# Kernel tuning notes

Hardware: AMD Instinct MI355X
Metric: run time of the kernel (lower is better)

Reference implementation:

```python
import jax, jax.numpy as jnp
import numpy as np

C_IN = 512      # in_channels
C1 = 256        # inter_channels (theta/phi)
C2 = 512        # context_channels (g) -- must equal C_IN (forward views with in_channels)
H = W = 97      # feature map size == hardcoded pos-encoding grid
POS = 97
BN_EPS = 1e-5


def _pos_encoding():
    """Faithful numpy port of _POSITION_ENCODEING_INIT_SINCOS(1, 97, 97, C_IN//2).
    Returns [1, C_IN, 97, 97] float32 (NCHW)."""
    d = C_IN // 2
    i = np.arange(d)
    div = np.power(10000.0, 2 * (i // 2) / d)            # [d]
    pos_x = np.linspace(0, 10, POS)                       # outer dim (dim 1 of NHWC)
    pos_y = np.linspace(0, 20, POS)                       # inner dim (dim 2 of NHWC)
    a = np.broadcast_to(pos_y[None, :, None] / div, (POS, POS, d))  # pos_y terms
    b = np.broadcast_to(pos_x[:, None, None] / div, (POS, POS, d))  # pos_x terms
    enc = np.concatenate([a, b], axis=-1).copy()          # [97, 97, 2d]
    enc[..., 0::2] = np.sin(enc[..., 0::2])
    enc[..., 1::2] = np.cos(enc[..., 1::2])
    return np.transpose(enc, (2, 0, 1)).astype(np.float32)[None]  # [1, C_IN, 97, 97]


def _conv1x1(x, w, b):
    # 1x1 conv as channel GEMM: w [O, C], x [B, C, H, W]
    return jnp.einsum('oc,bchw->bohw', w, x) + b[None, :, None, None]


def _bn_inf(x, gamma, beta):
    # InPlaceABNSync(activation='none') in inference: running_mean=0, running_var=1
    inv = (1.0 / np.sqrt(1.0 + BN_EPS)).astype(np.float32)
    return x * (gamma * inv)[None, :, None, None] + beta[None, :, None, None]


def setup_inputs() -> dict:
    key = jax.random.key(0)
    ks = jax.random.split(key, 8)
    s = 0.05
    return {
        'x':           jax.random.normal(ks[0], (1, C_IN, H, W), jnp.float32),
        'pos':         jnp.asarray(_pos_encoding()),                      # [1, C_IN, 97, 97]
        'w_theta':     jax.random.normal(ks[1], (C1, 2 * C_IN), jnp.float32) * s,
        'b_theta':     jax.random.normal(ks[2], (C1,), jnp.float32) * s,
        'gamma_theta': 1.0 + jax.random.normal(ks[3], (C1,), jnp.float32) * s,
        'beta_theta':  jax.random.normal(ks[4], (C1,), jnp.float32) * s,
        'w_g':         jax.random.normal(ks[5], (C2, 2 * C_IN), jnp.float32) * s,
        'b_g':         jax.random.normal(ks[6], (C2,), jnp.float32) * s,
        'w_out':       jax.random.normal(ks[7], (C_IN, C2), jnp.float32) * s,
        'b_out':       jnp.zeros((C_IN,), jnp.float32),
    }


def reference(x, pos, w_theta, b_theta, gamma_theta, beta_theta, w_g, b_g, w_out, b_out):
    B, _, h, w = x.shape
    c1 = w_theta.shape[0]
    c2 = w_g.shape[0]
    # concat fuse of input with (shared) positional encoding
    pos_b = jnp.broadcast_to(pos, (B,) + pos.shape[1:])
    x_mix = jnp.concatenate([x, pos_b], axis=1)                 # [B, 2C, H, W]
    # theta == phi (shared weights), so f = theta^T theta
    t = jax.nn.relu(_bn_inf(_conv1x1(x_mix, w_theta, b_theta), gamma_theta, beta_theta))
    tn = t.reshape(B, c1, h * w)                                # [B, c1, N]
    f = jnp.einsum('bcn,bcm->bnm', tn, tn) * (c1 ** -0.5)       # [B, N, N]
    G = jax.nn.softmax(f, axis=-1)
    g = _conv1x1(x_mix, w_g, b_g).reshape(B, c2, h * w)         # [B, c2, N]
    y = jnp.einsum('bnm,bcm->bcn', G, g).reshape(B, c2, h, w)   # value aggregation
    return _conv1x1(y, w_out, b_out)                            # [B, C_IN, H, W]
```

## Files before the change

### kernel.cpp

```cpp
#include <hip/hip_runtime.h>
#include <hip/hip_bf16.h>


#define NTOK 9409
#define NP   9472
#define C1V  256
#define C2V  512
#define KD   1024
#define BN_INV 0.9999950000374997f

typedef _Float16 f16;
typedef _Float16 f16x8 __attribute__((ext_vector_type(8)));
typedef _Float16 f16x4 __attribute__((ext_vector_type(4)));
typedef _Float16 f16x2 __attribute__((ext_vector_type(2)));
typedef float    f32x4 __attribute__((ext_vector_type(4)));

typedef const __attribute__((address_space(1))) unsigned int* gp_t;
typedef __attribute__((address_space(3))) unsigned int* lp_t;
#define GLOAD_LDS16(gsrc, ldst) \
  __builtin_amdgcn_global_load_lds((gp_t)(const void*)(gsrc), (lp_t)(void*)(ldst), 16, 0, 0)

__global__ __launch_bounds__(256) void cvt_w_kernel(
    const float* __restrict__ wt, const float* __restrict__ bt,
    const float* __restrict__ gam, const float* __restrict__ bet,
    const float* __restrict__ wg, const float* __restrict__ wo,
    f16* __restrict__ wt16, f16* __restrict__ wg16, f16* __restrict__ wo16,
    float* __restrict__ btf) {
  if (blockIdx.x == 1024) {
    int o = threadIdx.x;
    btf[o] = bt[o] * (gam[o] * BN_INV) + bet[o];
    return;
  }
  int i4 = (blockIdx.x * 256 + threadIdx.x) * 4;
  if (i4 < 262144) {
    float4 v = *(const float4*)(wt + i4);
    float s = gam[i4 >> 10] * BN_INV;
    f16x4 o; o[0]=(f16)(v.x*s); o[1]=(f16)(v.y*s); o[2]=(f16)(v.z*s); o[3]=(f16)(v.w*s);
    *(f16x4*)(wt16 + i4) = o;
  } else if (i4 < 262144 + 524288) {
    int j = i4 - 262144;
    float4 v = *(const float4*)(wg + j);
    f16x4 o; o[0]=(f16)v.x; o[1]=(f16)v.y; o[2]=(f16)v.z; o[3]=(f16)v.w;
    *(f16x4*)(wg16 + j) = o;
  } else {
    int j = i4 - 786432;
    float4 v = *(const float4*)(wo + j);
    f16x4 o; o[0]=(f16)v.x; o[1]=(f16)v.y; o[2]=(f16)v.z; o[3]=(f16)v.w;
    *(f16x4*)(wo16 + j) = o;
  }
}

__global__ __launch_bounds__(256) void xpose_kernel(
    const float* __restrict__ x, const float* __restrict__ pos,
    f16* __restrict__ xT) {
  __shared__ f16 tile[64 * 68];
  const int k0 = blockIdx.x * 64;
  const int n0 = blockIdx.y * 64;
  const int tid = threadIdx.x;
  {
    const int kl = tid >> 4;
    const int nl = (tid & 15) * 4;
#pragma unroll
    for (int i = 0; i < 4; ++i) {
      int k = k0 + i * 16 + kl;
      const float* src = (k < 512) ? (x + (size_t)k * NTOK) : (pos + (size_t)(k - 512) * NTOK);
#pragma unroll
      for (int dd = 0; dd < 4; ++dd) {
        int n = n0 + nl + dd;
        float v = (n < NTOK) ? src[n] : 0.f;
        tile[(nl + dd) * 68 + i * 16 + kl] = (f16)v;
      }
    }
  }
  __syncthreads();
  {
    const int nl = tid >> 2;
    const int kc = (tid & 3) * 16;
    const int n = n0 + nl;
    f16x4 a = *(const f16x4*)(tile + nl * 68 + kc);
    f16x4 b = *(const f16x4*)(tile + nl * 68 + kc + 4);
    f16x4 c = *(const f16x4*)(tile + nl * 68 + kc + 8);
    f16x4 d = *(const f16x4*)(tile + nl * 68 + kc + 12);
    f16x8 v0, v1;
#pragma unroll
    for (int jj = 0; jj < 4; ++jj) { v0[jj] = a[jj]; v0[4 + jj] = b[jj]; v1[jj] = c[jj]; v1[4 + jj] = d[jj]; }
    if (n >= NTOK) {
#pragma unroll
      for (int jj = 0; jj < 8; ++jj) { v0[jj] = (f16)0.f; v1[jj] = (f16)0.f; }
    }
    f16* dst = xT + (size_t)n * KD + k0 + kc;
    *(f16x8*)(dst) = v0;
    *(f16x8*)(dst + 8) = v1;
  }
}

__global__ __launch_bounds__(256) void proj_theta_kernel(
    const f16* __restrict__ xT, const f16* __restrict__ wt16,
    const float* __restrict__ btf, f16* __restrict__ tT) {
  const int n0 = blockIdx.x * 128;
  const int o0 = blockIdx.y * 64;
  const int tid = threadIdx.x;
  const int w = tid >> 6, lane = tid & 63, l15 = lane & 15, l4 = lane >> 4;
  const int nb = n0 + w * 32;
  f32x4 acc[2][4];
#pragma unroll
  for (int i = 0; i < 2; ++i)
#pragma unroll
    for (int j = 0; j < 4; ++j) acc[i][j] = (f32x4){0.f,0.f,0.f,0.f};
  const f16* ap0 = xT + (size_t)(nb + l15) * KD + l4 * 8;
  const f16* bp  = wt16 + (size_t)(o0 + l15) * KD + l4 * 8;
#pragma unroll 2
  for (int k0 = 0; k0 < KD; k0 += 32) {
    f16x8 a0 = *(const f16x8*)(ap0 + k0);
    f16x8 a1 = *(const f16x8*)(ap0 + 16 * KD + k0);
    f16x8 b[4];
#pragma unroll
    for (int fo = 0; fo < 4; ++fo) b[fo] = *(const f16x8*)(bp + fo * 16 * KD + k0);
#pragma unroll
    for (int fo = 0; fo < 4; ++fo) {
      acc[0][fo] = __builtin_amdgcn_mfma_f32_16x16x32_f16(a0, b[fo], acc[0][fo], 0, 0, 0);
      acc[1][fo] = __builtin_amdgcn_mfma_f32_16x16x32_f16(a1, b[fo], acc[1][fo], 0, 0, 0);
    }
  }
#pragma unroll
  for (int fm = 0; fm < 2; ++fm)
#pragma unroll
    for (int fo = 0; fo < 4; ++fo) {
      int o = o0 + fo * 16 + l15;
      float bb = btf[o];
#pragma unroll
      for (int j = 0; j < 4; ++j) {
        int n = nb + fm * 16 + l4 * 4 + j;
        tT[(size_t)n * C1V + o] = (f16)fmaxf(acc[fm][fo][j] + bb, 0.f);
      }
    }
}

__global__ __launch_bounds__(256) void proj_g_kernel(
    const f16* __restrict__ xT, const f16* __restrict__ wg16,
    const float* __restrict__ bg, f16* __restrict__ gc) {
  const int n0 = blockIdx.x * 128;
  const int c0 = blockIdx.y * 128;
  const int tid = threadIdx.x;
  const int w = tid >> 6, lane = tid & 63, l15 = lane & 15, l4 = lane >> 4;
  const int cb = c0 + (w >> 1) * 64, nb = n0 + (w & 1) * 64;
  f32x4 acc[4][4];
#pragma unroll
  for (int i = 0; i < 4; ++i)
#pragma unroll
    for (int j = 0; j < 4; ++j) acc[i][j] = (f32x4){0.f,0.f,0.f,0.f};
  const f16* ap = wg16 + (size_t)(cb + l15) * KD + l4 * 8;
  const f16* bp = xT + (size_t)(nb + l15) * KD + l4 * 8;
  for (int k0 = 0; k0 < KD; k0 += 32) {
    f16x8 a[4], b[4];
#pragma unroll
    for (int fc = 0; fc < 4; ++fc) a[fc] = *(const f16x8*)(ap + fc * 16 * KD + k0);
#pragma unroll
    for (int fn = 0; fn < 4; ++fn) b[fn] = *(const f16x8*)(bp + fn * 16 * KD + k0);
#pragma unroll
    for (int fc = 0; fc < 4; ++fc)
#pragma unroll
      for (int fn = 0; fn < 4; ++fn)
        acc[fc][fn] = __builtin_amdgcn_mfma_f32_16x16x32_f16(a[fc], b[fn], acc[fc][fn], 0, 0, 0);
  }
#pragma unroll
  for (int fc = 0; fc < 4; ++fc)
#pragma unroll
    for (int j = 0; j < 4; ++j) {
      int c = cb + fc * 16 + l4 * 4 + j;
      float bb = bg[c];
#pragma unroll
      for (int fn = 0; fn < 4; ++fn) {
        int n = nb + fn * 16 + l15;
        gc[(size_t)c * NP + n] = (f16)(acc[fc][fn][j] + bb);
      }
    }
}

__global__ __launch_bounds__(512, 2) void attn_kernel(
    const f16* __restrict__ tT, const f16* __restrict__ gc,
    f16* __restrict__ part, float* __restrict__ stats) {
  __shared__ char lds[65536 + 9216 + 1024];
  f16* Pb = (f16*)(lds + 65536);
  float* MhL = (float*)(lds + 65536 + 9216);
  float* LhL = (float*)(lds + 65536 + 9216 + 512);
  const int bid = blockIdx.x;
  const int rb = bid >> 2, q = bid & 3;
  const int tid = threadIdx.x;
  const int w = tid >> 6, lane = tid & 63, l15 = lane & 15, l4 = lane >> 4;
  const int wr = (w & 3) * 16;
  const int mh = w >> 2;
  const int cs = w * 64;

  f16x8 Qf[8];
  {
    const f16* qp = tT + (size_t)(rb * 64 + wr + l15) * C1V + l4 * 8;
#pragma unroll
    for (int kk = 0; kk < 8; ++kk) Qf[kk] = *(const f16x8*)(qp + kk * 32);
  }

  f32x4 acc[4][4];
#pragma unroll
  for (int cf = 0; cf < 4; ++cf)
#pragma unroll
    for (int rf = 0; rf < 4; ++rf) acc[cf][rf] = (f32x4){0.f,0.f,0.f,0.f};
  float Mq[4] = {-1e30f,-1e30f,-1e30f,-1e30f}, Lq[4] = {0.f,0.f,0.f,0.f};
  float Mp[4] = {-1e30f,-1e30f,-1e30f,-1e30f}, Lp[4] = {0.f,0.f,0.f,0.f};

#define KPREF(tt, dstbase)                                        \
  {                                                               \
    const f16* kb_ = tT + (size_t)(tt) * 64 * C1V;                \
    _Pragma("unroll")                                             \
    for (int i_ = 0; i_ < 4; ++i_) {                              \
      int m_ = w * 8 + i_ * 2 + (lane >> 5);                      \
      int s_ = lane & 31;                                         \
      GLOAD_LDS16(kb_ + m_ * C1V + ((s_ ^ (m_ & 7)) << 3),        \
                  (dstbase) + (w * 4 + i_) * 1024);               \
    }                                                             \
  }

  const int tt0 = q * 37;
  KPREF(tt0, lds)
  __syncthreads();

  const f16* vp = gc + (size_t)(cs + l15) * NP + l4 * 8;
  const int krow0 = (mh * 32 + l15) * 512;

  for (int ti = 0; ti < 37; ++ti) {
    const int tt = tt0 + ti;
    const int m0 = tt * 64;
    const int cur = ti & 1;
    f16x8 vf0[4], vf1[4];
#pragma unroll
    for (int cf = 0; cf < 4; ++cf) vf0[cf] = *(const f16x8*)(vp + (size_t)cf * 16 * NP + m0);
    if (ti + 1 < 37) KPREF(tt + 1, lds + (cur ^ 1) * 32768)
    const char* kbuf = lds + cur * 32768;
    f32x4 s0 = {0.f,0.f,0.f,0.f}, s1 = {0.f,0.f,0.f,0.f};
    __builtin_amdgcn_s_setprio(1);
#pragma unroll
    for (int kk = 0; kk < 8; ++kk) {
      int sl = ((kk * 4 + l4) ^ (l15 & 7)) << 4;
      f16x8 kb0 = *(const f16x8*)(kbuf + krow0 + sl);
      f16x8 kb1 = *(const f16x8*)(kbuf + krow0 + 8192 + sl);
      s0 = __builtin_amdgcn_mfma_f32_16x16x32_f16(Qf[kk], kb0, s0, 0, 0, 0);
      s1 = __builtin_amdgcn_mfma_f32_16x16x32_f16(Qf[kk], kb1, s1, 0, 0, 0);
    }
    __builtin_amdgcn_s_setprio(0);
    float sv0[4], sv1[4];
#pragma unroll
    for (int j = 0; j < 4; ++j) { sv0[j] = s0[j] * 0.0625f; sv1[j] = s1[j] * 0.0625f; }
    if (m0 + 64 > NTOK) {
      if (m0 + mh * 32 + l15 >= NTOK) {
#pragma unroll
        for (int j = 0; j < 4; ++j) sv0[j] = -1e30f;
      }
      if (m0 + mh * 32 + 16 + l15 >= NTOK) {
#pragma unroll
        for (int j = 0; j < 4; ++j) sv1[j] = -1e30f;
      }
    }
    float hm[4];
#pragma unroll
    for (int j = 0; j < 4; ++j) hm[j] = fmaxf(sv0[j], sv1[j]);
#pragma unroll
    for (int d = 1; d <= 8; d <<= 1)
#pragma unroll
      for (int j = 0; j < 4; ++j) hm[j] = fmaxf(hm[j], __shfl_xor(hm[j], d));
    if (l15 == 0) {
#pragma unroll
      for (int j = 0; j < 4; ++j) MhL[mh * 64 + wr + l4 * 4 + j] = hm[j];
    }
    asm volatile("s_waitcnt lgkmcnt(0)" ::: "memory");
    __builtin_amdgcn_s_barrier();
    __builtin_amdgcn_sched_barrier(0);
    float aq[4], ps[4];
#pragma unroll
    for (int j = 0; j < 4; ++j) {
      int gr = wr + l4 * 4 + j;
      float Mt = fmaxf(MhL[gr], MhL[64 + gr]);
      bool rs_ = Mt > Mq[j] + 8.f;
      aq[j] = rs_ ? __expf(Mq[j] - Mt) : 1.f;
      if (rs_) Mq[j] = Mt;
      float p0 = __expf(sv0[j] - Mq[j]);
      float p1 = __expf(sv1[j] - Mq[j]);
      Pb[gr * 72 + mh * 32 + l15] = (f16)p0;
      Pb[gr * 72 + mh * 32 + 16 + l15] = (f16)p1;
      ps[j] = p0 + p1;
    }
#pragma unroll
    for (int d = 1; d <= 8; d <<= 1)
#pragma unroll
      for (int j = 0; j < 4; ++j) ps[j] += __shfl_xor(ps[j], d);
    if (l15 == 0) {
#pragma unroll
      for (int j = 0; j < 4; ++j) LhL[mh * 64 + wr + l4 * 4 + j] = ps[j];
    }
    float ap[4];
    int anyp = 0;
#pragma unroll
    for (int rf = 0; rf < 4; ++rf) {
      int r = rf * 16 + l15;
      float Mt = fmaxf(MhL[r], MhL[64 + r]);
      bool rs_ = Mt > Mp[rf] + 8.f;
      ap[rf] = rs_ ? __expf(Mp[rf] - Mt) : 1.f;
      if (rs_) Mp[rf] = Mt;
      anyp |= (int)rs_;
    }
    if (__any(anyp)) {
#pragma unroll
      for (int cf = 0; cf < 4; ++cf)
#pragma unroll
        for (int rf = 0; rf < 4; ++rf)
#pragma unroll
          for (int j = 0; j < 4; ++j) acc[cf][rf][j] *= ap[rf];
    }
#pragma unroll
    for (int cf = 0; cf < 4; ++cf) vf1[cf] = *(const f16x8*)(vp + (size_t)cf * 16 * NP + m0 + 32);
    asm volatile("s_waitcnt vmcnt(4)" ::: "memory");
    asm volatile("s_waitcnt lgkmcnt(0)" ::: "memory");
    __builtin_amdgcn_s_barrier();
    __builtin_amdgcn_sched_barrier(0);
#pragma unroll
    for (int j = 0; j < 4; ++j) {
      int gr = wr + l4 * 4 + j;
      Lq[j] = Lq[j] * aq[j] + LhL[gr] + LhL[64 + gr];
    }
#pragma unroll
    for (int rf = 0; rf < 4; ++rf) {
      int r = rf * 16 + l15;
      Lp[rf] = Lp[rf] * ap[rf] + LhL[r] + LhL[64 + r];
    }
    __builtin_amdgcn_s_setprio(1);
    {
      f16x8 Pf[4];
#pragma unroll
      for (int rf = 0; rf < 4; ++rf)
        Pf[rf] = *(const f16x8*)((const char*)Pb + (rf * 16 + l15) * 144 + l4 * 16);
#pragma unroll
      for (int cf = 0; cf < 4; ++cf)
#pragma unroll
        for (int rf = 0; rf < 4; ++rf)
          acc[cf][rf] = __builtin_amdgcn_mfma_f32_16x16x32_f16(vf0[cf], Pf[rf], acc[cf][rf], 0, 0, 0);
#pragma unroll
      for (int rf = 0; rf < 4; ++rf)
        Pf[rf] = *(const f16x8*)((const char*)Pb + (rf * 16 + l15) * 144 + 64 + l4 * 16);
#pragma unroll
      for (int cf = 0; cf < 4; ++cf)
#pragma unroll
        for (int rf = 0; rf < 4; ++rf)
          acc[cf][rf] = __builtin_amdgcn_mfma_f32_16x16x32_f16(vf1[cf], Pf[rf], acc[cf][rf], 0, 0, 0);
    }
    __builtin_amdgcn_s_setprio(0);
  }
  float rinv[4];
#pragma unroll
  for (int rf = 0; rf < 4; ++rf) rinv[rf] = 1.0f / Lp[rf];
  const int prow = (rb * 4 + q) * 64;
  if (mh == 0 && l15 == 0) {
#pragma unroll
    for (int j = 0; j < 4; ++j) {
      int gr = wr + l4 * 4 + j;
      stats[(prow + gr) * 2] = Mq[j];
      stats[(prow + gr) * 2 + 1] = Lq[j];
    }
  }
#pragma unroll
  for (int cf = 0; cf < 4; ++cf)
#pragma unroll
    for (int rf = 0; rf < 4; ++rf) {
      f16x4 st;
#pragma unroll
      for (int j = 0; j < 4; ++j) st[j] = (f16)(acc[cf][rf][j] * rinv[rf]);
      *(f16x4*)(part + (size_t)(prow + rf * 16 + l15) * C2V + cs + cf * 16 + l4 * 4) = st;
    }
#undef KPREF
}

__global__ __launch_bounds__(256) void merge_kernel(
    const f16* __restrict__ part, const float* __restrict__ stats,
    f16* __restrict__ yT) {
  const int n = blockIdx.x;
  const int rb = n >> 6, rl = n & 63;
  float Mq[4], Lq[4];
#pragma unroll
  for (int qq = 0; qq < 4; ++qq) {
    int pr = (rb * 4 + qq) * 64 + rl;
    Mq[qq] = stats[pr * 2];
    Lq[qq] = stats[pr * 2 + 1];
  }
  float Ms = fmaxf(fmaxf(Mq[0], Mq[1]), fmaxf(Mq[2], Mq[3]));
  float wq[4], lt = 0.f;
#pragma unroll
  for (int qq = 0; qq < 4; ++qq) { wq[qq] = __expf(Mq[qq] - Ms) * Lq[qq]; lt += wq[qq]; }
  float inv = 1.f / lt;
  const int c = threadIdx.x * 2;
  float y0 = 0.f, y1 = 0.f;
#pragma unroll
  for (int qq = 0; qq < 4; ++qq) {
    f16x2 v = *(const f16x2*)(part + (size_t)((rb * 4 + qq) * 64 + rl) * C2V + c);
    y0 += wq[qq] * (float)v[0];
    y1 += wq[qq] * (float)v[1];
  }
  f16x2 o; o[0] = (f16)(y0 * inv); o[1] = (f16)(y1 * inv);
  *(f16x2*)(yT + (size_t)n * C2V + c) = o;
}

__global__ __launch_bounds__(256) void out_gemm_kernel(
    const f16* __restrict__ yT, const f16* __restrict__ wo16,
    const float* __restrict__ bo, float* __restrict__ out) {
  const int n0 = blockIdx.x * 128;
  const int o0 = blockIdx.y * 128;
  const int tid = threadIdx.x;
  const int w = tid >> 6, lane = tid & 63, l15 = lane & 15, l4 = lane >> 4;
  const int ob = o0 + (w >> 1) * 64, nb = n0 + (w & 1) * 64;
  f32x4 acc[4][4];
#pragma unroll
  for (int i = 0; i < 4; ++i)
#pragma unroll
    for (int j = 0; j < 4; ++j) acc[i][j] = (f32x4){0.f,0.f,0.f,0.f};
  const f16* ap = wo16 + (size_t)(ob + l15) * C2V + l4 * 8;
  const f16* bp = yT + (size_t)(nb + l15) * C2V + l4 * 8;
  for (int k0 = 0; k0 < C2V; k0 += 32) {
    f16x8 a[4], b[4];
#pragma unroll
    for (int fc = 0; fc < 4; ++fc) a[fc] = *(const f16x8*)(ap + fc * 16 * C2V + k0);
#pragma unroll
    for (int fn = 0; fn < 4; ++fn) b[fn] = *(const f16x8*)(bp + fn * 16 * C2V + k0);
#pragma unroll
    for (int fc = 0; fc < 4; ++fc)
#pragma unroll
      for (int fn = 0; fn < 4; ++fn)
        acc[fc][fn] = __builtin_amdgcn_mfma_f32_16x16x32_f16(a[fc], b[fn], acc[fc][fn], 0, 0, 0);
  }
#pragma unroll
  for (int fn = 0; fn < 4; ++fn) {
    int n = nb + fn * 16 + l15;
    if (n >= NTOK) continue;
#pragma unroll
    for (int fc = 0; fc < 4; ++fc)
#pragma unroll
      for (int j = 0; j < 4; ++j) {
        int o = ob + fc * 16 + l4 * 4 + j;
        out[(size_t)o * NTOK + n] = acc[fc][fn][j] + bo[o];
      }
  }
}

extern "C" void kernel_launch(void* const* d_in, const int* in_sizes, int n_in,
                              void* d_out, int out_size, void* d_ws, size_t ws_size,
                              hipStream_t stream) {
  const float* x   = (const float*)d_in[0];
  const float* pos = (const float*)d_in[1];
  const float* wt  = (const float*)d_in[2];
  const float* bt  = (const float*)d_in[3];
  const float* gam = (const float*)d_in[4];
  const float* bet = (const float*)d_in[5];
  const float* wg  = (const float*)d_in[6];
  const float* bg  = (const float*)d_in[7];
  const float* wo  = (const float*)d_in[8];
  const float* bo  = (const float*)d_in[9];
  float* out = (float*)d_out;

  char* ws = (char*)d_ws;
  f16*   tT    = (f16*)(ws + 0);
  f16*   gc    = (f16*)(ws + 4849664);
  f16*   wt16  = (f16*)(ws + 14548992);
  f16*   wg16  = (f16*)(ws + 15073280);
  f16*   wo16  = (f16*)(ws + 16121856);
  float* btf   = (float*)(ws + 16646144);
  float* stats = (float*)(ws + 16647168);
  f16*   yT    = (f16*)(ws + 16950272);
  f16*   part  = (f16*)(ws + 26649600);
  f16*   xT    = (f16*)(ws + 26649600);

  cvt_w_kernel<<<1025, 256, 0, stream>>>(wt, bt, gam, bet, wg, wo, wt16, wg16, wo16, btf);
  xpose_kernel<<<dim3(16, 148), 256, 0, stream>>>(x, pos, xT);
  proj_theta_kernel<<<dim3(74, 4), 256, 0, stream>>>(xT, wt16, btf, tT);
  proj_g_kernel<<<dim3(74, 4), 256, 0, stream>>>(xT, wg16, bg, gc);
  attn_kernel<<<592, 512, 0, stream>>>(tT, gc, part, stats);
  merge_kernel<<<NTOK, 256, 0, stream>>>(part, stats, yT);
  out_gemm_kernel<<<dim3(74, 4), 256, 0, stream>>>(yT, wo16, bo, out);
}
```

Measured before the change: 618.3 us.

## Restructure attention kernel to 32-row query tiles with per-wave local softmax

The attention kernel is rebuilt around 32 query rows and 32 key tiles per step with 256-thread blocks and more blocks (1180). Each wave computes S transposed, does its softmax max and sum with two shuffles, and merges pairs through a small double-buffered LDS exchange, which drops one of the two block barriers per tile. The 1/sqrt(c1) scale is folded into the theta projection (0.25 on the f16 output), and padded tokens are zeroed there. The merge kernel is adapted to the new 32-row partial layout. The trade-offs are smaller tiles with less K/V reuse per block, lower precision from rescaling P in f16, and more work in the merge step.

```diff
diff --git a/kernel.cpp b/kernel.cpp
--- a/kernel.cpp
+++ b/kernel.cpp
@@ -131,7 +131,8 @@
 #pragma unroll
       for (int j = 0; j < 4; ++j) {
         int n = nb + fm * 16 + l4 * 4 + j;
-        tT[(size_t)n * C1V + o] = (f16)fmaxf(acc[fm][fo][j] + bb, 0.f);
+        float v = (n < NTOK) ? 0.25f * fmaxf(acc[fm][fo][j] + bb, 0.f) : 0.f;
+        tT[(size_t)n * C1V + o] = (f16)v;
       }
     }
 }
@@ -177,214 +178,187 @@
     }
 }
 
-__global__ __launch_bounds__(512, 2) void attn_kernel(
+__global__ __launch_bounds__(256, 3) void attn_kernel(
     const f16* __restrict__ tT, const f16* __restrict__ gc,
     f16* __restrict__ part, float* __restrict__ stats) {
-  __shared__ char lds[65536 + 9216 + 1024];
-  f16* Pb = (f16*)(lds + 65536);
-  float* MhL = (float*)(lds + 65536 + 9216);
-  float* LhL = (float*)(lds + 65536 + 9216 + 512);
+  __shared__ char lds[32768 + 5120 + 1024];
   const int bid = blockIdx.x;
-  const int rb = bid >> 2, q = bid & 3;
+  const int q = bid & 3;
   const int tid = threadIdx.x;
   const int w = tid >> 6, lane = tid & 63, l15 = lane & 15, l4 = lane >> 4;
-  const int wr = (w & 3) * 16;
-  const int mh = w >> 2;
-  const int cs = w * 64;
+  const int qr = w & 1, qm = w >> 1;
+  const int cs = w * 128;
 
   f16x8 Qf[8];
   {
-    const f16* qp = tT + (size_t)(rb * 64 + wr + l15) * C1V + l4 * 8;
+    const f16* qp = tT + (size_t)((bid >> 2) * 32 + qr * 16 + l15) * C1V + l4 * 8;
 #pragma unroll
     for (int kk = 0; kk < 8; ++kk) Qf[kk] = *(const f16x8*)(qp + kk * 32);
   }
-
-  f32x4 acc[4][4];
-#pragma unroll
-  for (int cf = 0; cf < 4; ++cf)
-#pragma unroll
-    for (int rf = 0; rf < 4; ++rf) acc[cf][rf] = (f32x4){0.f,0.f,0.f,0.f};
-  float Mq[4] = {-1e30f,-1e30f,-1e30f,-1e30f}, Lq[4] = {0.f,0.f,0.f,0.f};
-  float Mp[4] = {-1e30f,-1e30f,-1e30f,-1e30f}, Lp[4] = {0.f,0.f,0.f,0.f};
+  const int mloc = qm * 16 + l15;
+  const int kkx = (mloc >> 2) & 1;
+  const int kbase = mloc * 512 + ((l4 ^ (mloc & 3)) << 4);
+  int soff[4];
+#pragma unroll
+  for (int i = 0; i < 4; ++i) {
+    int m_ = i * 8 + (tid >> 5), s_ = tid & 31;
+    soff[i] = m_ * C1V + ((s_ ^ (m_ & 7)) << 3);
+  }
+  const int sdst = tid * 16;
+  const f16* vp = gc + (size_t)(cs + l15) * NP + l4 * 8;
+
+  f32x4 acc[8][2];
+#pragma unroll
+  for (int cf = 0; cf < 8; ++cf)
+#pragma unroll
+    for (int rf = 0; rf < 2; ++rf) acc[cf][rf] = (f32x4){0.f,0.f,0.f,0.f};
+  float Mr[2] = {-1e30f, -1e30f}, Lr[2] = {0.f, 0.f};
 
 #define KPREF(tt, dstbase)                                        \
   {                                                               \
-    const f16* kb_ = tT + (size_t)(tt) * 64 * C1V;                \
+    const f16* kb_ = tT + (size_t)(tt) * 32 * C1V;                \
     _Pragma("unroll")                                             \
-    for (int i_ = 0; i_ < 4; ++i_) {                              \
-      int m_ = w * 8 + i_ * 2 + (lane >> 5);                      \
-      int s_ = lane & 31;                                         \
-      GLOAD_LDS16(kb_ + m_ * C1V + ((s_ ^ (m_ & 7)) << 3),        \
-                  (dstbase) + (w * 4 + i_) * 1024);               \
-    }                                                             \
-  }
-
-  const int tt0 = q * 37;
+    for (int i_ = 0; i_ < 4; ++i_)                                \
+      GLOAD_LDS16(kb_ + soff[i_], (dstbase) + i_ * 4096 + sdst);  \
+  }
+
+  const int tt0 = q * 74;
   KPREF(tt0, lds)
-  __syncthreads();
-
-  const f16* vp = gc + (size_t)(cs + l15) * NP + l4 * 8;
-  const int krow0 = (mh * 32 + l15) * 512;
-
-  for (int ti = 0; ti < 37; ++ti) {
+  asm volatile("s_waitcnt vmcnt(0)" ::: "memory");
+  __builtin_amdgcn_s_barrier();
+
+  for (int ti = 0; ti < 74; ++ti) {
     const int tt = tt0 + ti;
-    const int m0 = tt * 64;
+    const int m0 = tt * 32;
     const int cur = ti & 1;
-    f16x8 vf0[4], vf1[4];
-#pragma unroll
-    for (int cf = 0; cf < 4; ++cf) vf0[cf] = *(const f16x8*)(vp + (size_t)cf * 16 * NP + m0);
-    if (ti + 1 < 37) KPREF(tt + 1, lds + (cur ^ 1) * 32768)
-    const char* kbuf = lds + cur * 32768;
-    f32x4 s0 = {0.f,0.f,0.f,0.f}, s1 = {0.f,0.f,0.f,0.f};
+    char* Pb = lds + 32768 + cur * 2560;
+    char* mlb = lds + 32768 + 5120 + cur * 512;
+    if (ti + 1 < 74) KPREF(tt + 1, lds + (cur ^ 1) * 16384)
+    __builtin_amdgcn_sched_barrier(0);
+    f16x8 vfA[4];
+#pragma unroll
+    for (int cf = 0; cf < 4; ++cf)
+      vfA[cf] = *(const f16x8*)(vp + (size_t)cf * 16 * NP + m0);
+    const char* kbuf = lds + cur * 16384;
+    f32x4 s0 = {0.f,0.f,0.f,0.f};
     __builtin_amdgcn_s_setprio(1);
 #pragma unroll
     for (int kk = 0; kk < 8; ++kk) {
-      int sl = ((kk * 4 + l4) ^ (l15 & 7)) << 4;
-      f16x8 kb0 = *(const f16x8*)(kbuf + krow0 + sl);
-      f16x8 kb1 = *(const f16x8*)(kbuf + krow0 + 8192 + sl);
-      s0 = __builtin_amdgcn_mfma_f32_16x16x32_f16(Qf[kk], kb0, s0, 0, 0, 0);
-      s1 = __builtin_amdgcn_mfma_f32_16x16x32_f16(Qf[kk], kb1, s1, 0, 0, 0);
+      f16x8 kf = *(const f16x8*)(kbuf + kbase + ((kk ^ kkx) << 6));
+      s0 = __builtin_amdgcn_mfma_f32_16x16x32_f16(kf, Qf[kk], s0, 0, 0, 0);
     }
     __builtin_amdgcn_s_setprio(0);
-    float sv0[4], sv1[4];
-#pragma unroll
-    for (int j = 0; j < 4; ++j) { sv0[j] = s0[j] * 0.0625f; sv1[j] = s1[j] * 0.0625f; }
-    if (m0 + 64 > NTOK) {
-      if (m0 + mh * 32 + l15 >= NTOK) {
-#pragma unroll
-        for (int j = 0; j < 4; ++j) sv0[j] = -1e30f;
-      }
-      if (m0 + mh * 32 + 16 + l15 >= NTOK) {
-#pragma unroll
-        for (int j = 0; j < 4; ++j) sv1[j] = -1e30f;
-      }
-    }
-    float hm[4];
-#pragma unroll
-    for (int j = 0; j < 4; ++j) hm[j] = fmaxf(sv0[j], sv1[j]);
-#pragma unroll
-    for (int d = 1; d <= 8; d <<= 1)
-#pragma unroll
-      for (int j = 0; j < 4; ++j) hm[j] = fmaxf(hm[j], __shfl_xor(hm[j], d));
-    if (l15 == 0) {
-#pragma unroll
-      for (int j = 0; j < 4; ++j) MhL[mh * 64 + wr + l4 * 4 + j] = hm[j];
-    }
-    asm volatile("s_waitcnt lgkmcnt(0)" ::: "memory");
-    __builtin_amdgcn_s_barrier();
-    __builtin_amdgcn_sched_barrier(0);
-    float aq[4], ps[4];
-#pragma unroll
-    for (int j = 0; j < 4; ++j) {
-      int gr = wr + l4 * 4 + j;
-      float Mt = fmaxf(MhL[gr], MhL[64 + gr]);
-      bool rs_ = Mt > Mq[j] + 8.f;
-      aq[j] = rs_ ? __expf(Mq[j] - Mt) : 1.f;
-      if (rs_) Mq[j] = Mt;
-      float p0 = __expf(sv0[j] - Mq[j]);
-      float p1 = __expf(sv1[j] - Mq[j]);
-      Pb[gr * 72 + mh * 32 + l15] = (f16)p0;
-      Pb[gr * 72 + mh * 32 + 16 + l15] = (f16)p1;
-      ps[j] = p0 + p1;
-    }
-#pragma unroll
-    for (int d = 1; d <= 8; d <<= 1)
-#pragma unroll
-      for (int j = 0; j < 4; ++j) ps[j] += __shfl_xor(ps[j], d);
-    if (l15 == 0) {
-#pragma unroll
-      for (int j = 0; j < 4; ++j) LhL[mh * 64 + wr + l4 * 4 + j] = ps[j];
-    }
-    float ap[4];
-    int anyp = 0;
-#pragma unroll
-    for (int rf = 0; rf < 4; ++rf) {
-      int r = rf * 16 + l15;
-      float Mt = fmaxf(MhL[r], MhL[64 + r]);
-      bool rs_ = Mt > Mp[rf] + 8.f;
-      ap[rf] = rs_ ? __expf(Mp[rf] - Mt) : 1.f;
-      if (rs_) Mp[rf] = Mt;
-      anyp |= (int)rs_;
-    }
-    if (__any(anyp)) {
-#pragma unroll
-      for (int cf = 0; cf < 4; ++cf)
-#pragma unroll
-        for (int rf = 0; rf < 4; ++rf)
-#pragma unroll
-          for (int j = 0; j < 4; ++j) acc[cf][rf][j] *= ap[rf];
-    }
-#pragma unroll
-    for (int cf = 0; cf < 4; ++cf) vf1[cf] = *(const f16x8*)(vp + (size_t)cf * 16 * NP + m0 + 32);
+    float sv[4];
+#pragma unroll
+    for (int j = 0; j < 4; ++j) sv[j] = s0[j];
+    if (m0 + 32 > NTOK) {
+#pragma unroll
+      for (int j = 0; j < 4; ++j)
+        if (m0 + qm * 16 + l4 * 4 + j >= NTOK) sv[j] = -1e30f;
+    }
+    float mx = fmaxf(fmaxf(sv[0], sv[1]), fmaxf(sv[2], sv[3]));
+    mx = fmaxf(mx, __shfl_xor(mx, 16));
+    mx = fmaxf(mx, __shfl_xor(mx, 32));
+    float p[4], ls = 0.f;
+#pragma unroll
+    for (int j = 0; j < 4; ++j) { p[j] = __expf(sv[j] - mx); ls += p[j]; }
+    ls += __shfl_xor(ls, 16);
+    ls += __shfl_xor(ls, 32);
+    {
+      f16x4 pw;
+#pragma unroll
+      for (int j = 0; j < 4; ++j) pw[j] = (f16)p[j];
+      *(f16x4*)(Pb + (qr * 16 + l15) * 80 + qm * 32 + l4 * 8) = pw;
+      if (l4 == 0) *(float2*)(mlb + (qm * 32 + qr * 16 + l15) * 8) = make_float2(mx, ls);
+    }
     asm volatile("s_waitcnt vmcnt(4)" ::: "memory");
     asm volatile("s_waitcnt lgkmcnt(0)" ::: "memory");
     __builtin_amdgcn_s_barrier();
     __builtin_amdgcn_sched_barrier(0);
-#pragma unroll
-    for (int j = 0; j < 4; ++j) {
-      int gr = wr + l4 * 4 + j;
-      Lq[j] = Lq[j] * aq[j] + LhL[gr] + LhL[64 + gr];
-    }
-#pragma unroll
-    for (int rf = 0; rf < 4; ++rf) {
-      int r = rf * 16 + l15;
-      Lp[rf] = Lp[rf] * ap[rf] + LhL[r] + LhL[64 + r];
+    f16x8 vfB[4];
+#pragma unroll
+    for (int cf = 0; cf < 4; ++cf)
+      vfB[cf] = *(const f16x8*)(vp + (size_t)(cf + 4) * 16 * NP + m0);
+    float mlx[2], mll[2], mox[2], mol[2], Mn[2];
+    int grow = 0;
+#pragma unroll
+    for (int rf = 0; rf < 2; ++rf) {
+      float2 mlv = *(const float2*)(mlb + ((l4 >> 1) * 32 + rf * 16 + l15) * 8);
+      mlx[rf] = mlv.x; mll[rf] = mlv.y;
+      mox[rf] = __shfl_xor(mlv.x, 32);
+      mol[rf] = __shfl_xor(mlv.y, 32);
+      float mx2 = fmaxf(mlx[rf], mox[rf]);
+      Mn[rf] = (mx2 > Mr[rf] + 8.f) ? mx2 : Mr[rf];
+      grow |= (Mn[rf] != Mr[rf]) ? 1 : 0;
+    }
+    if (__any(grow)) {
+#pragma unroll
+      for (int rf = 0; rf < 2; ++rf) {
+        float a = __expf(Mr[rf] - Mn[rf]);
+        Mr[rf] = Mn[rf];
+        Lr[rf] *= a;
+#pragma unroll
+        for (int cf = 0; cf < 8; ++cf)
+#pragma unroll
+          for (int j = 0; j < 4; ++j) acc[cf][rf][j] *= a;
+      }
+    }
+    f16x8 Pf[2];
+#pragma unroll
+    for (int rf = 0; rf < 2; ++rf) {
+      float ah = __expf(mlx[rf] - Mr[rf]);
+      float ao = __expf(mox[rf] - Mr[rf]);
+      Lr[rf] += ah * mll[rf] + ao * mol[rf];
+      Pf[rf] = *(const f16x8*)(Pb + (rf * 16 + l15) * 80 + l4 * 16);
+      f16 ah16 = (f16)ah;
+#pragma unroll
+      for (int e = 0; e < 8; ++e) Pf[rf][e] *= ah16;
     }
     __builtin_amdgcn_s_setprio(1);
-    {
-      f16x8 Pf[4];
-#pragma unroll
-      for (int rf = 0; rf < 4; ++rf)
-        Pf[rf] = *(const f16x8*)((const char*)Pb + (rf * 16 + l15) * 144 + l4 * 16);
-#pragma unroll
-      for (int cf = 0; cf < 4; ++cf)
-#pragma unroll
-        for (int rf = 0; rf < 4; ++rf)
-          acc[cf][rf] = __builtin_amdgcn_mfma_f32_16x16x32_f16(vf0[cf], Pf[rf], acc[cf][rf], 0, 0, 0);
-#pragma unroll
-      for (int rf = 0; rf < 4; ++rf)
-        Pf[rf] = *(const f16x8*)((const char*)Pb + (rf * 16 + l15) * 144 + 64 + l4 * 16);
-#pragma unroll
-      for (int cf = 0; cf < 4; ++cf)
-#pragma unroll
-        for (int rf = 0; rf < 4; ++rf)
-          acc[cf][rf] = __builtin_amdgcn_mfma_f32_16x16x32_f16(vf1[cf], Pf[rf], acc[cf][rf], 0, 0, 0);
-    }
+#pragma unroll
+    for (int cf = 0; cf < 4; ++cf)
+#pragma unroll
+      for (int rf = 0; rf < 2; ++rf)
+        acc[cf][rf] = __builtin_amdgcn_mfma_f32_16x16x32_f16(vfA[cf], Pf[rf], acc[cf][rf], 0, 0, 0);
+#pragma unroll
+    for (int cf = 0; cf < 4; ++cf)
+#pragma unroll
+      for (int rf = 0; rf < 2; ++rf)
+        acc[cf + 4][rf] = __builtin_amdgcn_mfma_f32_16x16x32_f16(vfB[cf], Pf[rf], acc[cf + 4][rf], 0, 0, 0);
     __builtin_amdgcn_s_setprio(0);
   }
-  float rinv[4];
-#pragma unroll
-  for (int rf = 0; rf < 4; ++rf) rinv[rf] = 1.0f / Lp[rf];
-  const int prow = (rb * 4 + q) * 64;
-  if (mh == 0 && l15 == 0) {
-#pragma unroll
-    for (int j = 0; j < 4; ++j) {
-      int gr = wr + l4 * 4 + j;
-      stats[(prow + gr) * 2] = Mq[j];
-      stats[(prow + gr) * 2 + 1] = Lq[j];
-    }
-  }
-#pragma unroll
-  for (int cf = 0; cf < 4; ++cf)
-#pragma unroll
-    for (int rf = 0; rf < 4; ++rf) {
+#undef KPREF
+  float rinv[2];
+#pragma unroll
+  for (int rf = 0; rf < 2; ++rf) rinv[rf] = 1.0f / Lr[rf];
+  const int prow = bid * 32;
+  if (w == 0 && l4 == 0) {
+#pragma unroll
+    for (int rf = 0; rf < 2; ++rf) {
+      stats[(prow + rf * 16 + l15) * 2] = Mr[rf];
+      stats[(prow + rf * 16 + l15) * 2 + 1] = Lr[rf];
+    }
+  }
+#pragma unroll
+  for (int cf = 0; cf < 8; ++cf)
+#pragma unroll
+    for (int rf = 0; rf < 2; ++rf) {
       f16x4 st;
 #pragma unroll
       for (int j = 0; j < 4; ++j) st[j] = (f16)(acc[cf][rf][j] * rinv[rf]);
       *(f16x4*)(part + (size_t)(prow + rf * 16 + l15) * C2V + cs + cf * 16 + l4 * 4) = st;
     }
-#undef KPREF
 }
 
 __global__ __launch_bounds__(256) void merge_kernel(
     const f16* __restrict__ part, const float* __restrict__ stats,
     f16* __restrict__ yT) {
   const int n = blockIdx.x;
-  const int rb = n >> 6, rl = n & 63;
+  const int rb = n >> 5, rl = n & 31;
   float Mq[4], Lq[4];
 #pragma unroll
   for (int qq = 0; qq < 4; ++qq) {
-    int pr = (rb * 4 + qq) * 64 + rl;
+    int pr = (rb * 4 + qq) * 32 + rl;
     Mq[qq] = stats[pr * 2];
     Lq[qq] = stats[pr * 2 + 1];
   }
@@ -397,7 +371,7 @@
   float y0 = 0.f, y1 = 0.f;
 #pragma unroll
   for (int qq = 0; qq < 4; ++qq) {
-    f16x2 v = *(const f16x2*)(part + (size_t)((rb * 4 + qq) * 64 + rl) * C2V + c);
+    f16x2 v = *(const f16x2*)(part + (size_t)((rb * 4 + qq) * 32 + rl) * C2V + c);
     y0 += wq[qq] * (float)v[0];
     y1 += wq[qq] * (float)v[1];
   }
@@ -477,7 +451,7 @@
   xpose_kernel<<<dim3(16, 148), 256, 0, stream>>>(x, pos, xT);
   proj_theta_kernel<<<dim3(74, 4), 256, 0, stream>>>(xT, wt16, btf, tT);
   proj_g_kernel<<<dim3(74, 4), 256, 0, stream>>>(xT, wg16, bg, gc);
-  attn_kernel<<<592, 512, 0, stream>>>(tT, gc, part, stats);
+  attn_kernel<<<1180, 256, 0, stream>>>(tT, gc, part, stats);
   merge_kernel<<<NTOK, 256, 0, stream>>>(part, stats, yT);
   out_gemm_kernel<<<dim3(74, 4), 256, 0, stream>>>(yT, wo16, bo, out);
 }
```

After: 760.9 us. +23.1%, slower.
